# Kernel tuning notes

Measured on AMD Instinct MI355X. Metric: run time of the kernel, lower is better.

Reference implementation:

```python
import jax, jax.numpy as jnp
import numpy as np

D_LOGIC = 256
D_MEMORY = 256
NHEAD = 4
B, S = 2, 4096


def setup_inputs() -> dict:
    key = jax.random.key(0)
    ks = jax.random.split(key, 12)
    scale = 0.02
    x_logic = jax.random.normal(ks[0], (B, S, D_LOGIC), dtype=jnp.float32)
    x_memory = jax.random.normal(ks[1], (B, S, D_MEMORY), dtype=jnp.float32)
    mask = jax.random.randint(ks[2], (1, 1, S, S), 0, 2, dtype=jnp.int32)
    # torch nn.Linear weights are [out_features, in_features]
    Wq = jax.random.normal(ks[3], (D_LOGIC, D_LOGIC), dtype=jnp.float32) * scale
    bq = jnp.zeros((D_LOGIC,), dtype=jnp.float32)
    Wk = jax.random.normal(ks[4], (D_LOGIC, D_LOGIC), dtype=jnp.float32) * scale
    bk = jnp.zeros((D_LOGIC,), dtype=jnp.float32)
    Wv = jax.random.normal(ks[5], (D_MEMORY, D_MEMORY), dtype=jnp.float32) * scale
    bv = jnp.zeros((D_MEMORY,), dtype=jnp.float32)
    Wo = jax.random.normal(ks[6], (D_MEMORY, D_MEMORY), dtype=jnp.float32) * scale
    bo = jnp.zeros((D_MEMORY,), dtype=jnp.float32)
    return {"x_logic": x_logic, "x_memory": x_memory, "mask": mask,
            "Wq": Wq, "bq": bq, "Wk": Wk, "bk": bk,
            "Wv": Wv, "bv": bv, "Wo": Wo, "bo": bo}


def reference(x_logic, x_memory, mask, Wq, bq, Wk, bk, Wv, bv, Wo, bo):
    batch, seq, _ = x_logic.shape
    hd_l = D_LOGIC // NHEAD   # head_dim_logic
    hd_m = D_MEMORY // NHEAD  # head_dim_memory
    # Q, K from logic stream
    Q = (x_logic @ Wq.T + bq).reshape(batch, seq, NHEAD, hd_l)
    K = (x_logic @ Wk.T + bk).reshape(batch, seq, NHEAD, hd_l)
    # scores: [B, H, S, S]
    scores = jnp.einsum('bqhd,bkhd->bhqk', Q, K) / jnp.sqrt(jnp.float32(hd_l))
    scores = jnp.where(mask == 0, jnp.float32(-1e9), scores)
    attn = jax.nn.softmax(scores, axis=-1)
    # V from memory stream
    V = (x_memory @ Wv.T + bv).reshape(batch, seq, NHEAD, hd_m)
    out = jnp.einsum('bhqk,bkhd->bqhd', attn, V).reshape(batch, seq, D_MEMORY)
    return out @ Wo.T + bo
```

## Files before the change

### kernel.cpp

```cpp
#include <hip/hip_runtime.h>

#define S_  4096
#define HD_ 64
#define H_  4
#define B_  2
#define DM  256
#define NS  4
#define KSPAN (S_ / NS)
#define NITER (KSPAN / 64)

typedef __bf16 bf16x8 __attribute__((ext_vector_type(8)));
typedef __bf16 bf16x4 __attribute__((ext_vector_type(4)));
typedef float  f32x4  __attribute__((ext_vector_type(4)));
typedef unsigned long long u64;

__device__ __forceinline__ bf16x8 cvt8(const float* p) {
    float4 u0 = *reinterpret_cast<const float4*>(p);
    float4 u1 = *reinterpret_cast<const float4*>(p + 4);
    bf16x8 r = { (__bf16)u0.x, (__bf16)u0.y, (__bf16)u0.z, (__bf16)u0.w,
                 (__bf16)u1.x, (__bf16)u1.y, (__bf16)u1.z, (__bf16)u1.w };
    return r;
}

__global__ __launch_bounds__(256) void pack_kernel(const int* __restrict__ mask,
                                                   u64* __restrict__ packed,
                                                   const float* __restrict__ Wq,
                                                   const float* __restrict__ Wk,
                                                   const float* __restrict__ Wv,
                                                   const float* __restrict__ Wo,
                                                   __bf16* __restrict__ wqb,
                                                   __bf16* __restrict__ wkb,
                                                   __bf16* __restrict__ wvb,
                                                   __bf16* __restrict__ wob) {
    const int bid = blockIdx.x;
    if (bid < 1024) {
        const int gw   = bid * 4 + (threadIdx.x >> 6);
        const int lane = threadIdx.x & 63;
        const int r  = lane >> 4;
        const int ll = lane & 15;
#pragma unroll
        for (int sb = 0; sb < 4; ++sb) {
            int4 v[4];
#pragma unroll
            for (int j = 0; j < 4; ++j) {
                const int u   = gw + (sb * 4 + j) * 4096;
                const int kbb = u & 63;
                const int q0  = (u >> 6) * 4;
                v[j] = *reinterpret_cast<const int4*>(
                    mask + (size_t)(q0 + r) * S_ + kbb * 64 + ll * 4);
            }
#pragma unroll
            for (int j = 0; j < 4; ++j) {
                const int u   = gw + (sb * 4 + j) * 4096;
                const int kbb = u & 63;
                const int q0  = (u >> 6) * 4;
                const u64 b0 = __ballot(v[j].x != 0);
                const u64 b1 = __ballot(v[j].y != 0);
                const u64 b2 = __ballot(v[j].z != 0);
                const u64 b3 = __ballot(v[j].w != 0);
                if (ll == 0) {
                    const u64 word = ((b0 >> (16 * r)) & 0xFFFFull)
                                   | (((b1 >> (16 * r)) & 0xFFFFull) << 16)
                                   | (((b2 >> (16 * r)) & 0xFFFFull) << 32)
                                   | (((b3 >> (16 * r)) & 0xFFFFull) << 48);
                    packed[(size_t)kbb * S_ + q0 + r] = word;
                }
            }
        }
        return;
    }
    const int t = (bid - 1024) * 256 + threadIdx.x;
#pragma unroll
    for (int j = 0; j < 4; ++j) {
        const int idx = t + j * 16384;
        const int arr = idx >> 14, k = idx & 16383;
        const float* src = arr == 0 ? Wq : arr == 1 ? Wk : arr == 2 ? Wv : Wo;
        __bf16* dst      = arr == 0 ? wqb : arr == 1 ? wkb : arr == 2 ? wvb : wob;
        float4 v = reinterpret_cast<const float4*>(src)[k];
        bf16x4 o = { (__bf16)v.x, (__bf16)v.y, (__bf16)v.z, (__bf16)v.w };
        reinterpret_cast<bf16x4*>(dst)[k] = o;
    }
}

__global__ __launch_bounds__(256) void proj_qkv_kernel(const float* __restrict__ xl,
                                                       const float* __restrict__ xm,
                                                       const __bf16* __restrict__ wqb,
                                                       const __bf16* __restrict__ wkb,
                                                       const __bf16* __restrict__ wvb,
                                                       const float* __restrict__ bq,
                                                       const float* __restrict__ bk,
                                                       const float* __restrict__ bv,
                                                       __bf16* __restrict__ Qb,
                                                       __bf16* __restrict__ Kb,
                                                       __bf16* __restrict__ Vtb) {
    const int mode = blockIdx.z;
    const int ny   = blockIdx.y;
    const float*  X    = (mode == 2) ? xm : xl;
    const __bf16* W    = (mode == 0) ? wqb : (mode == 1) ? wkb : wvb;
    const float*  bias = (mode == 0) ? bq : (mode == 1) ? bk : bv;
    const float scale  = (mode == 0) ? 0.18033688011112042f : 1.0f;

    const int wid  = threadIdx.x >> 6;
    const int lane = threadIdx.x & 63;
    const int g = lane >> 4, c = lane & 15;
    const int m0 = blockIdx.x * 64 + wid * 16;
    const float* Xp = X + (size_t)m0 * DM;

    f32x4 acc[8];
#pragma unroll
    for (int i = 0; i < 8; ++i) acc[i] = (f32x4){0.f, 0.f, 0.f, 0.f};

#pragma unroll
    for (int kf = 0; kf < 8; ++kf) {
        bf16x8 a = cvt8(Xp + c * DM + kf * 32 + g * 8);
#pragma unroll
        for (int nt = 0; nt < 8; ++nt) {
            bf16x8 b = *reinterpret_cast<const bf16x8*>(
                W + (size_t)(ny * 128 + nt * 16 + c) * DM + kf * 32 + g * 8);
            acc[nt] = __builtin_amdgcn_mfma_f32_16x16x32_bf16(a, b, acc[nt], 0, 0, 0);
        }
    }

#pragma unroll
    for (int nt = 0; nt < 8; ++nt) {
        const int n = ny * 128 + nt * 16 + c;
        const float bs = bias[n];
        const int h = n >> 6, d = n & 63;
#pragma unroll
        for (int r = 0; r < 4; ++r) {
            const int m = m0 + g * 4 + r;
            const float v = (acc[nt][r] + bs) * scale;
            const int b_ = m >> 12, s = m & (S_ - 1);
            if (mode == 0)
                Qb[((size_t)(b_ * H_ + h) * S_ + s) * HD_ + d] = (__bf16)v;
            else if (mode == 1)
                Kb[((size_t)(b_ * H_ + h) * S_ + s) * HD_ + d] = (__bf16)v;
            else
                Vtb[((size_t)(b_ * H_ + h) * HD_ + d) * S_ + s] = (__bf16)v;
        }
    }
}

__global__ __launch_bounds__(256, 4) void attn_kernel(const __bf16* __restrict__ Q,
                                                      const __bf16* __restrict__ K,
                                                      const __bf16* __restrict__ Vt,
                                                      const u64* __restrict__ packed,
                                                      __bf16* __restrict__ Opart,
                                                      float* __restrict__ Lpart) {
    __shared__ __bf16 Kt[64][72];
    __shared__ __bf16 Vl[64][72];
    __shared__ __bf16 Pl[4][32][72];

    const int bh = blockIdx.x;
    const int sp = blockIdx.y;
    const int qt = blockIdx.z;
    const int tid  = threadIdx.x;
    const int wid  = tid >> 6;
    const int lane = tid & 63;
    const int g = lane >> 4, c = lane & 15;
    const int q0w = qt * 128 + wid * 32;

    const __bf16* Qp = Q + ((size_t)bh * S_ + q0w) * HD_;
    bf16x8 qb[2][2];
#pragma unroll
    for (int qh = 0; qh < 2; ++qh) {
        qb[qh][0] = *reinterpret_cast<const bf16x8*>(Qp + (qh * 16 + c) * HD_ + g * 8);
        qb[qh][1] = *reinterpret_cast<const bf16x8*>(Qp + (qh * 16 + c) * HD_ + 32 + g * 8);
    }

    const __bf16* Kp = K  + (size_t)bh * S_ * HD_;
    const __bf16* Vp = Vt + (size_t)bh * HD_ * S_;

    const int srow = tid >> 2;
    const int sseg = (tid & 3) * 16;

    f32x4 o[2][4];
#pragma unroll
    for (int qh = 0; qh < 2; ++qh)
#pragma unroll
        for (int i = 0; i < 4; ++i) o[qh][i] = (f32x4){0.f, 0.f, 0.f, 0.f};
    float rs[2] = {0.f, 0.f};

    const int k0 = sp * KSPAN;

    bf16x8 kr0, kr1, vr0, vr1;
    {
        const __bf16* krow = Kp + (size_t)(k0 + srow) * HD_ + sseg;
        const __bf16* vrow = Vp + (size_t)srow * S_ + k0 + sseg;
        kr0 = *reinterpret_cast<const bf16x8*>(krow);
        kr1 = *reinterpret_cast<const bf16x8*>(krow + 8);
        vr0 = *reinterpret_cast<const bf16x8*>(vrow);
        vr1 = *reinterpret_cast<const bf16x8*>(vrow + 8);
        *reinterpret_cast<bf16x8*>(&Kt[srow][sseg])     = kr0;
        *reinterpret_cast<bf16x8*>(&Kt[srow][sseg + 8]) = kr1;
        *reinterpret_cast<bf16x8*>(&Vl[srow][sseg])     = vr0;
        *reinterpret_cast<bf16x8*>(&Vl[srow][sseg + 8]) = vr1;
    }
    __syncthreads();

    for (int it = 0; it < NITER; ++it) {
        const int kb = k0 + it * 64;
        const bool more = (it + 1 < NITER);
        if (more) {
            const __bf16* krow = Kp + (size_t)(kb + 64 + srow) * HD_ + sseg;
            const __bf16* vrow = Vp + (size_t)srow * S_ + kb + 64 + sseg;
            kr0 = *reinterpret_cast<const bf16x8*>(krow);
            kr1 = *reinterpret_cast<const bf16x8*>(krow + 8);
            vr0 = *reinterpret_cast<const bf16x8*>(vrow);
            vr1 = *reinterpret_cast<const bf16x8*>(vrow + 8);
        }

        const u64 mwA = packed[(size_t)(kb >> 6) * S_ + q0w + c];
        const u64 mwB = packed[(size_t)(kb >> 6) * S_ + q0w + 16 + c];

        f32x4 st[4][2];
#pragma unroll
        for (int nt = 0; nt < 4; ++nt) {
            bf16x8 ka0 = *reinterpret_cast<const bf16x8*>(&Kt[nt * 16 + c][g * 8]);
            bf16x8 ka1 = *reinterpret_cast<const bf16x8*>(&Kt[nt * 16 + c][32 + g * 8]);
#pragma unroll
            for (int qh = 0; qh < 2; ++qh) {
                f32x4 z = (f32x4){0.f, 0.f, 0.f, 0.f};
                st[nt][qh] = __builtin_amdgcn_mfma_f32_16x16x32_bf16(ka0, qb[qh][0], z, 0, 0, 0);
                st[nt][qh] = __builtin_amdgcn_mfma_f32_16x16x32_bf16(ka1, qb[qh][1], st[nt][qh], 0, 0, 0);
            }
        }

#pragma unroll
        for (int qh = 0; qh < 2; ++qh) {
            const u64 mw = qh ? mwB : mwA;
            const unsigned wlo = (unsigned)mw, whi = (unsigned)(mw >> 32);
#pragma unroll
            for (int nt = 0; nt < 4; ++nt) {
                const unsigned sh = nt * 4 + g;
                float p0 = ((wlo >> sh) & 1u)        ? exp2f(st[nt][qh][0]) : 0.f;
                float p1 = ((wlo >> (sh + 16)) & 1u) ? exp2f(st[nt][qh][1]) : 0.f;
                float p2 = ((whi >> sh) & 1u)        ? exp2f(st[nt][qh][2]) : 0.f;
                float p3 = ((whi >> (sh + 16)) & 1u) ? exp2f(st[nt][qh][3]) : 0.f;
                rs[qh] += (p0 + p1) + (p2 + p3);
                bf16x4 pw = { (__bf16)p0, (__bf16)p1, (__bf16)p2, (__bf16)p3 };
                *reinterpret_cast<bf16x4*>(&Pl[wid][qh * 16 + c][nt * 16 + g * 4]) = pw;
            }
        }

        bf16x8 pa[2][2];
#pragma unroll
        for (int qh = 0; qh < 2; ++qh) {
            pa[qh][0] = *reinterpret_cast<const bf16x8*>(&Pl[wid][qh * 16 + c][g * 8]);
            pa[qh][1] = *reinterpret_cast<const bf16x8*>(&Pl[wid][qh * 16 + c][32 + g * 8]);
        }

#pragma unroll
        for (int nt = 0; nt < 4; ++nt) {
            bf16x8 vb0 = *reinterpret_cast<const bf16x8*>(&Vl[nt * 16 + c][g * 8]);
            bf16x8 vb1 = *reinterpret_cast<const bf16x8*>(&Vl[nt * 16 + c][32 + g * 8]);
#pragma unroll
            for (int qh = 0; qh < 2; ++qh) {
                o[qh][nt] = __builtin_amdgcn_mfma_f32_16x16x32_bf16(pa[qh][0], vb0, o[qh][nt], 0, 0, 0);
                o[qh][nt] = __builtin_amdgcn_mfma_f32_16x16x32_bf16(pa[qh][1], vb1, o[qh][nt], 0, 0, 0);
            }
        }

        __syncthreads();
        if (more) {
            *reinterpret_cast<bf16x8*>(&Kt[srow][sseg])     = kr0;
            *reinterpret_cast<bf16x8*>(&Kt[srow][sseg + 8]) = kr1;
            *reinterpret_cast<bf16x8*>(&Vl[srow][sseg])     = vr0;
            *reinterpret_cast<bf16x8*>(&Vl[srow][sseg + 8]) = vr1;
            __syncthreads();
        }
    }

#pragma unroll
    for (int qh = 0; qh < 2; ++qh) {
        rs[qh] += __shfl_xor(rs[qh], 16);
        rs[qh] += __shfl_xor(rs[qh], 32);
    }
    if (lane < 16) {
        Lpart[(size_t)(bh * NS + sp) * S_ + q0w + c]      = rs[0];
        Lpart[(size_t)(bh * NS + sp) * S_ + q0w + 16 + c] = rs[1];
    }

#pragma unroll
    for (int qh = 0; qh < 2; ++qh) {
        const size_t obase = ((size_t)(bh * NS + sp) * S_ + q0w + qh * 16) * 64;
#pragma unroll
        for (int nt = 0; nt < 4; ++nt) {
#pragma unroll
            for (int r = 0; r < 4; ++r)
                Opart[obase + (size_t)(g * 4 + r) * 64 + nt * 16 + c] = (__bf16)o[qh][nt][r];
        }
    }
}

__global__ __launch_bounds__(256) void proj_o_kernel(const __bf16* __restrict__ Opart,
                                                     const float* __restrict__ Lpart,
                                                     const __bf16* __restrict__ wob,
                                                     const float* __restrict__ bo,
                                                     float* __restrict__ out) {
    const int ny   = blockIdx.y;
    const int wid  = threadIdx.x >> 6;
    const int lane = threadIdx.x & 63;
    const int g = lane >> 4, c = lane & 15;
    const int m0 = blockIdx.x * 64 + wid * 16;

    const int row = m0 + c;
    const int b_ = row >> 12, s = row & (S_ - 1);

    f32x4 acc[8];
#pragma unroll
    for (int i = 0; i < 8; ++i) acc[i] = (f32x4){0.f, 0.f, 0.f, 0.f};

#pragma unroll
    for (int kf = 0; kf < 8; ++kf) {
        const int dcol = kf * 32 + g * 8;
        const int h = dcol >> 6, dm = dcol & 63;
        const int bh = b_ * H_ + h;
        float l = 0.f;
        float sum[8] = {0.f, 0.f, 0.f, 0.f, 0.f, 0.f, 0.f, 0.f};
#pragma unroll
        for (int sp = 0; sp < NS; ++sp) {
            l += Lpart[(size_t)(bh * NS + sp) * S_ + s];
            const size_t base = ((size_t)(bh * NS + sp) * S_ + s) * 64 + dm;
            bf16x8 p = *reinterpret_cast<const bf16x8*>(Opart + base);
#pragma unroll
            for (int j = 0; j < 8; ++j) sum[j] += (float)p[j];
        }
        const float invl = 1.0f / l;
        bf16x8 a = { (__bf16)(sum[0] * invl), (__bf16)(sum[1] * invl),
                     (__bf16)(sum[2] * invl), (__bf16)(sum[3] * invl),
                     (__bf16)(sum[4] * invl), (__bf16)(sum[5] * invl),
                     (__bf16)(sum[6] * invl), (__bf16)(sum[7] * invl) };
#pragma unroll
        for (int nt = 0; nt < 8; ++nt) {
            bf16x8 b = *reinterpret_cast<const bf16x8*>(
                wob + (size_t)(ny * 128 + nt * 16 + c) * DM + kf * 32 + g * 8);
            acc[nt] = __builtin_amdgcn_mfma_f32_16x16x32_bf16(a, b, acc[nt], 0, 0, 0);
        }
    }

#pragma unroll
    for (int nt = 0; nt < 8; ++nt) {
        const int n = ny * 128 + nt * 16 + c;
        const float bs = bo[n];
#pragma unroll
        for (int r = 0; r < 4; ++r) {
            const int m = m0 + g * 4 + r;
            out[(size_t)m * DM + n] = acc[nt][r] + bs;
        }
    }
}

extern "C" void kernel_launch(void* const* d_in, const int* in_sizes, int n_in,
                              void* d_out, int out_size, void* d_ws, size_t ws_size,
                              hipStream_t stream) {
    const float* x_logic  = (const float*)d_in[0];
    const float* x_memory = (const float*)d_in[1];
    const int*   mask     = (const int*)d_in[2];
    const float* Wq = (const float*)d_in[3];
    const float* bq = (const float*)d_in[4];
    const float* Wk = (const float*)d_in[5];
    const float* bk = (const float*)d_in[6];
    const float* Wv = (const float*)d_in[7];
    const float* bv = (const float*)d_in[8];
    const float* Wo = (const float*)d_in[9];
    const float* bo = (const float*)d_in[10];
    float* out = (float*)d_out;

    char* ws = (char*)d_ws;
    size_t off = 0;
    auto alloc = [&](size_t bytes) { char* p = ws + off; off += (bytes + 255) & ~255ull; return p; };

    const size_t NX = (size_t)B_ * S_ * DM;
    u64*    packed = (u64*)alloc((size_t)S_ * (S_ / 64) * 8);
    __bf16* wqb = (__bf16*)alloc((size_t)DM * DM * 2);
    __bf16* wkb = (__bf16*)alloc((size_t)DM * DM * 2);
    __bf16* wvb = (__bf16*)alloc((size_t)DM * DM * 2);
    __bf16* wob = (__bf16*)alloc((size_t)DM * DM * 2);
    __bf16* Qb  = (__bf16*)alloc(NX * 2);
    __bf16* Kb  = (__bf16*)alloc(NX * 2);
    __bf16* Vtb = (__bf16*)alloc(NX * 2);
    __bf16* Opart = (__bf16*)alloc((size_t)B_ * H_ * NS * S_ * HD_ * 2);
    float*  Lpart = (float*)alloc((size_t)B_ * H_ * NS * S_ * 4);

    pack_kernel<<<1088, 256, 0, stream>>>(mask, packed, Wq, Wk, Wv, Wo, wqb, wkb, wvb, wob);
    proj_qkv_kernel<<<dim3(128, 2, 3), 256, 0, stream>>>(x_logic, x_memory, wqb, wkb, wvb,
                                                         bq, bk, bv, Qb, Kb, Vtb);
    attn_kernel<<<dim3(8, NS, 32), 256, 0, stream>>>(Qb, Kb, Vtb, packed, Opart, Lpart);
    proj_o_kernel<<<dim3(128, 2), 256, 0, stream>>>(Opart, Lpart, wob, bo, out);
}
```

Baseline: 135.0 us.

## Fuse mask packing with QKV projection and transpose P via permlane swaps

Merges the mask-packing/weight-conversion kernel with the QKV projection kernel into a single launch. The projection now converts fp32 weights to bf16 on the fly instead of reading pre-converted copies. In the attention kernel, the P tile is no longer bounced through shared memory; it is rearranged into the MFMA A-operand layout with v_permlane32/16_swap instructions, removing LDS writes and reads plus the shared buffer. This saves a launch and LDS traffic, but costs extra fp32 weight loads and conversions per projection block, and it depends on the permlane lane mapping being correct.

```diff
diff --git a/kernel.cpp b/kernel.cpp
--- a/kernel.cpp
+++ b/kernel.cpp
@@ -12,6 +12,7 @@
 typedef __bf16 bf16x8 __attribute__((ext_vector_type(8)));
 typedef __bf16 bf16x4 __attribute__((ext_vector_type(4)));
 typedef float  f32x4  __attribute__((ext_vector_type(4)));
+typedef unsigned u32x4 __attribute__((ext_vector_type(4)));
 typedef unsigned long long u64;
 
 __device__ __forceinline__ bf16x8 cvt8(const float* p) {
@@ -22,16 +23,27 @@
     return r;
 }
 
-__global__ __launch_bounds__(256) void pack_kernel(const int* __restrict__ mask,
-                                                   u64* __restrict__ packed,
-                                                   const float* __restrict__ Wq,
-                                                   const float* __restrict__ Wk,
-                                                   const float* __restrict__ Wv,
-                                                   const float* __restrict__ Wo,
-                                                   __bf16* __restrict__ wqb,
-                                                   __bf16* __restrict__ wkb,
-                                                   __bf16* __restrict__ wvb,
-                                                   __bf16* __restrict__ wob) {
+__device__ __forceinline__ unsigned pk2(float a, float b) {
+    unsigned la = (unsigned)__builtin_bit_cast(unsigned short, (__bf16)a);
+    unsigned lb = (unsigned)__builtin_bit_cast(unsigned short, (__bf16)b);
+    return la | (lb << 16);
+}
+
+__global__ __launch_bounds__(256) void fused_prep_kernel(const int* __restrict__ mask,
+                                                         u64* __restrict__ packed,
+                                                         const float* __restrict__ xl,
+                                                         const float* __restrict__ xm,
+                                                         const float* __restrict__ Wq,
+                                                         const float* __restrict__ Wk,
+                                                         const float* __restrict__ Wv,
+                                                         const float* __restrict__ Wo,
+                                                         const float* __restrict__ bq,
+                                                         const float* __restrict__ bk,
+                                                         const float* __restrict__ bv,
+                                                         __bf16* __restrict__ Qb,
+                                                         __bf16* __restrict__ Kb,
+                                                         __bf16* __restrict__ Vtb,
+                                                         __bf16* __restrict__ wob) {
     const int bid = blockIdx.x;
     if (bid < 1024) {
         const int gw   = bid * 4 + (threadIdx.x >> 6);
@@ -69,41 +81,30 @@
         }
         return;
     }
-    const int t = (bid - 1024) * 256 + threadIdx.x;
-#pragma unroll
-    for (int j = 0; j < 4; ++j) {
-        const int idx = t + j * 16384;
-        const int arr = idx >> 14, k = idx & 16383;
-        const float* src = arr == 0 ? Wq : arr == 1 ? Wk : arr == 2 ? Wv : Wo;
-        __bf16* dst      = arr == 0 ? wqb : arr == 1 ? wkb : arr == 2 ? wvb : wob;
-        float4 v = reinterpret_cast<const float4*>(src)[k];
-        bf16x4 o = { (__bf16)v.x, (__bf16)v.y, (__bf16)v.z, (__bf16)v.w };
-        reinterpret_cast<bf16x4*>(dst)[k] = o;
-    }
-}
-
-__global__ __launch_bounds__(256) void proj_qkv_kernel(const float* __restrict__ xl,
-                                                       const float* __restrict__ xm,
-                                                       const __bf16* __restrict__ wqb,
-                                                       const __bf16* __restrict__ wkb,
-                                                       const __bf16* __restrict__ wvb,
-                                                       const float* __restrict__ bq,
-                                                       const float* __restrict__ bk,
-                                                       const float* __restrict__ bv,
-                                                       __bf16* __restrict__ Qb,
-                                                       __bf16* __restrict__ Kb,
-                                                       __bf16* __restrict__ Vtb) {
-    const int mode = blockIdx.z;
-    const int ny   = blockIdx.y;
+    if (bid >= 1792) {
+        const int t = (bid - 1792) * 256 + threadIdx.x;
+#pragma unroll
+        for (int j = 0; j < 4; ++j) {
+            const int k = t + j * 4096;
+            float4 v = reinterpret_cast<const float4*>(Wo)[k];
+            bf16x4 o = { (__bf16)v.x, (__bf16)v.y, (__bf16)v.z, (__bf16)v.w };
+            reinterpret_cast<bf16x4*>(wob)[k] = o;
+        }
+        return;
+    }
+    const int pb   = bid - 1024;
+    const int mode = pb >> 8;
+    const int mb   = (pb & 255) >> 1;
+    const int ny   = pb & 1;
     const float*  X    = (mode == 2) ? xm : xl;
-    const __bf16* W    = (mode == 0) ? wqb : (mode == 1) ? wkb : wvb;
+    const float*  W    = (mode == 0) ? Wq : (mode == 1) ? Wk : Wv;
     const float*  bias = (mode == 0) ? bq : (mode == 1) ? bk : bv;
     const float scale  = (mode == 0) ? 0.18033688011112042f : 1.0f;
 
     const int wid  = threadIdx.x >> 6;
     const int lane = threadIdx.x & 63;
     const int g = lane >> 4, c = lane & 15;
-    const int m0 = blockIdx.x * 64 + wid * 16;
+    const int m0 = mb * 64 + wid * 16;
     const float* Xp = X + (size_t)m0 * DM;
 
     f32x4 acc[8];
@@ -115,8 +116,7 @@
         bf16x8 a = cvt8(Xp + c * DM + kf * 32 + g * 8);
 #pragma unroll
         for (int nt = 0; nt < 8; ++nt) {
-            bf16x8 b = *reinterpret_cast<const bf16x8*>(
-                W + (size_t)(ny * 128 + nt * 16 + c) * DM + kf * 32 + g * 8);
+            bf16x8 b = cvt8(W + (size_t)(ny * 128 + nt * 16 + c) * DM + kf * 32 + g * 8);
             acc[nt] = __builtin_amdgcn_mfma_f32_16x16x32_bf16(a, b, acc[nt], 0, 0, 0);
         }
     }
@@ -149,7 +149,6 @@
                                                       float* __restrict__ Lpart) {
     __shared__ __bf16 Kt[64][72];
     __shared__ __bf16 Vl[64][72];
-    __shared__ __bf16 Pl[4][32][72];
 
     const int bh = blockIdx.x;
     const int sp = blockIdx.y;
@@ -226,10 +225,12 @@
             }
         }
 
+        bf16x8 pa[2][2];
 #pragma unroll
         for (int qh = 0; qh < 2; ++qh) {
             const u64 mw = qh ? mwB : mwA;
             const unsigned wlo = (unsigned)mw, whi = (unsigned)(mw >> 32);
+            unsigned W[4][2];
 #pragma unroll
             for (int nt = 0; nt < 4; ++nt) {
                 const unsigned sh = nt * 4 + g;
@@ -238,16 +239,25 @@
                 float p2 = ((whi >> sh) & 1u)        ? exp2f(st[nt][qh][2]) : 0.f;
                 float p3 = ((whi >> (sh + 16)) & 1u) ? exp2f(st[nt][qh][3]) : 0.f;
                 rs[qh] += (p0 + p1) + (p2 + p3);
-                bf16x4 pw = { (__bf16)p0, (__bf16)p1, (__bf16)p2, (__bf16)p3 };
-                *reinterpret_cast<bf16x4*>(&Pl[wid][qh * 16 + c][nt * 16 + g * 4]) = pw;
-            }
-        }
-
-        bf16x8 pa[2][2];
-#pragma unroll
-        for (int qh = 0; qh < 2; ++qh) {
-            pa[qh][0] = *reinterpret_cast<const bf16x8*>(&Pl[wid][qh * 16 + c][g * 8]);
-            pa[qh][1] = *reinterpret_cast<const bf16x8*>(&Pl[wid][qh * 16 + c][32 + g * 8]);
+                W[nt][0] = pk2(p0, p1);
+                W[nt][1] = pk2(p2, p3);
+            }
+            unsigned a0 = W[0][0], b0 = W[1][0];
+            asm("v_permlane32_swap_b32 %0, %1" : "+v"(a0), "+v"(b0));
+            asm("v_permlane16_swap_b32 %0, %1" : "+v"(a0), "+v"(b0));
+            unsigned a1 = W[0][1], b1 = W[1][1];
+            asm("v_permlane32_swap_b32 %0, %1" : "+v"(a1), "+v"(b1));
+            asm("v_permlane16_swap_b32 %0, %1" : "+v"(a1), "+v"(b1));
+            u32x4 w0 = { a0, a1, b0, b1 };
+            pa[qh][0] = __builtin_bit_cast(bf16x8, w0);
+            unsigned a2 = W[2][0], b2 = W[3][0];
+            asm("v_permlane32_swap_b32 %0, %1" : "+v"(a2), "+v"(b2));
+            asm("v_permlane16_swap_b32 %0, %1" : "+v"(a2), "+v"(b2));
+            unsigned a3 = W[2][1], b3 = W[3][1];
+            asm("v_permlane32_swap_b32 %0, %1" : "+v"(a3), "+v"(b3));
+            asm("v_permlane16_swap_b32 %0, %1" : "+v"(a3), "+v"(b3));
+            u32x4 w1 = { a2, a3, b2, b3 };
+            pa[qh][1] = __builtin_bit_cast(bf16x8, w1);
         }
 
 #pragma unroll
@@ -373,9 +383,6 @@
 
     const size_t NX = (size_t)B_ * S_ * DM;
     u64*    packed = (u64*)alloc((size_t)S_ * (S_ / 64) * 8);
-    __bf16* wqb = (__bf16*)alloc((size_t)DM * DM * 2);
-    __bf16* wkb = (__bf16*)alloc((size_t)DM * DM * 2);
-    __bf16* wvb = (__bf16*)alloc((size_t)DM * DM * 2);
     __bf16* wob = (__bf16*)alloc((size_t)DM * DM * 2);
     __bf16* Qb  = (__bf16*)alloc(NX * 2);
     __bf16* Kb  = (__bf16*)alloc(NX * 2);
@@ -383,9 +390,9 @@
     __bf16* Opart = (__bf16*)alloc((size_t)B_ * H_ * NS * S_ * HD_ * 2);
     float*  Lpart = (float*)alloc((size_t)B_ * H_ * NS * S_ * 4);
 
-    pack_kernel<<<1088, 256, 0, stream>>>(mask, packed, Wq, Wk, Wv, Wo, wqb, wkb, wvb, wob);
-    proj_qkv_kernel<<<dim3(128, 2, 3), 256, 0, stream>>>(x_logic, x_memory, wqb, wkb, wvb,
-                                                         bq, bk, bv, Qb, Kb, Vtb);
+    fused_prep_kernel<<<1808, 256, 0, stream>>>(mask, packed, x_logic, x_memory,
+                                                Wq, Wk, Wv, Wo, bq, bk, bv,
+                                                Qb, Kb, Vtb, wob);
     attn_kernel<<<dim3(8, NS, 32), 256, 0, stream>>>(Qb, Kb, Vtb, packed, Opart, Lpart);
     proj_o_kernel<<<dim3(128, 2), 256, 0, stream>>>(Opart, Lpart, wob, bo, out);
 }
```

Result: slower. 211.3 us (+56.5%).
